# Performance work log

Hardware: AMD Instinct MI355X
Metric: run time of the kernel (lower is better)

The kernel has to match this reference:

```python
import jax, jax.numpy as jnp
import numpy as np

N, E, D_IN, H, C = 100000, 1600000, 256, 128, 10


def setup_inputs() -> dict:
    key = jax.random.key(0)
    ks = jax.random.split(key, 12)
    x = jax.random.normal(ks[0], (N, D_IN), dtype=jnp.float32)
    edge_index = jax.random.randint(ks[1], (2, E), 0, N, dtype=jnp.int64)
    reranker_scores = jax.random.normal(ks[2], (N,), dtype=jnp.float32)
    s_in = 1.0 / np.sqrt(D_IN)
    s_h = 1.0 / np.sqrt(H)
    # SAGEConv: lin_l applies to aggregated neighbors (with bias), lin_r to root (no bias)
    W_l = jax.random.uniform(ks[3], (H, D_IN), jnp.float32, -s_in, s_in)
    b_l = jax.random.uniform(ks[4], (H,), jnp.float32, -s_in, s_in)
    W_r = jax.random.uniform(ks[5], (H, D_IN), jnp.float32, -s_in, s_in)
    W_res = jax.random.uniform(ks[6], (H, D_IN), jnp.float32, -s_in, s_in)
    b_res = jax.random.uniform(ks[7], (H,), jnp.float32, -s_in, s_in)
    W_score = jax.random.uniform(ks[8], (1, H), jnp.float32, -s_h, s_h)
    b_score = jax.random.uniform(ks[9], (1,), jnp.float32, -s_h, s_h)
    W_crit = jax.random.uniform(ks[10], (C, H), jnp.float32, -s_h, s_h)
    b_crit = jax.random.uniform(ks[11], (C,), jnp.float32, -s_h, s_h)
    alpha = jnp.float32(0.65)
    return {"x": x, "edge_index": edge_index, "reranker_scores": reranker_scores,
            "W_l": W_l, "b_l": b_l, "W_r": W_r, "W_res": W_res, "b_res": b_res,
            "W_score": W_score, "b_score": b_score, "W_crit": W_crit, "b_crit": b_crit,
            "alpha": alpha}


def reference(x, edge_index, reranker_scores, W_l, b_l, W_r, W_res, b_res,
              W_score, b_score, W_crit, b_crit, alpha):
    src, dst = edge_index[0], edge_index[1]
    n = x.shape[0]
    ones = jnp.ones(src.shape[0], dtype=x.dtype)
    deg = jax.ops.segment_sum(ones, dst, num_segments=n)          # [N]
    nbr_sum = jax.ops.segment_sum(x[src], dst, num_segments=n)    # [N, D_IN]
    agg = nbr_sum / jnp.maximum(deg, 1.0)[:, None]                # mean aggregation
    # SAGEConv: lin_l(agg) + lin_r(x); relu; dropout (eval -> identity); residual
    h = jax.nn.relu(agg @ W_l.T + b_l + x @ W_r.T)                # [N, H]
    h = h + (x @ W_res.T + b_res)                                 # residual projection
    gnn_scores = (h @ W_score.T + b_score)[:, 0]                  # [N]
    a = jax.nn.sigmoid(alpha)
    final_scores = a * reranker_scores + (1.0 - a) * gnn_scores
    criterion_logits = h @ W_crit.T + b_crit                      # [N, C]
    return final_scores, criterion_logits
```

## Files before the change

### kernel.cpp

```cpp
#include <hip/hip_runtime.h>
#include <math.h>

#define DIN 256
#define HDIM 128
#define NCRIT 10
#define BSH 9
#define EPB 4096

typedef __bf16 bf16;
typedef bf16 bf16x8 __attribute__((ext_vector_type(8)));
typedef float f32x4 __attribute__((ext_vector_type(4)));
typedef float f32x2 __attribute__((ext_vector_type(2)));

static inline size_t alignup(size_t x, size_t a) { return (x + a - 1) & ~(a - 1); }

__device__ inline float bflo(unsigned v) { return __uint_as_float(v << 16); }
__device__ inline float bfhi(unsigned v) { return __uint_as_float(v & 0xffff0000u); }

__device__ inline bf16x8 cvt8(float4 v0, float4 v1) {
    bf16x8 w;
    w[0] = (bf16)v0.x; w[1] = (bf16)v0.y; w[2] = (bf16)v0.z; w[3] = (bf16)v0.w;
    w[4] = (bf16)v1.x; w[5] = (bf16)v1.y; w[6] = (bf16)v1.z; w[7] = (bf16)v1.w;
    return w;
}

__device__ inline void gl_lds16(const void* g, void* l) {
    __builtin_amdgcn_global_load_lds(
        (const __attribute__((address_space(1))) unsigned*)g,
        (__attribute__((address_space(3))) unsigned*)l, 16, 0, 0);
}

__global__ __launch_bounds__(256) void k_bucket2(
    const int* __restrict__ src, const int* __restrict__ dst, int E,
    int* __restrict__ bcnt, int2* __restrict__ bpool, int capb, int nB,
    const float* __restrict__ Wl, const float* __restrict__ Wr,
    const float* __restrict__ Wres,
    const float* __restrict__ wscore, const float* __restrict__ wcrit,
    const float* __restrict__ bres, const float* __restrict__ bscore,
    const float* __restrict__ bcrit,
    bf16* __restrict__ WcatT, float* __restrict__ cq)
{
    int t = threadIdx.x;
    int b = blockIdx.x;
    if (b < 64) {
        int base = (b * 256 + t) * 4;
        int r = base >> 8;
        int c0 = base & 255;
        const float* W = (r < 128) ? Wl : Wr;
        float4 v = *(const float4*)&W[(size_t)(r & 127) * 256 + c0];
        bf16 o[4] = {(bf16)v.x, (bf16)v.y, (bf16)v.z, (bf16)v.w};
        char* d = (char*)WcatT + ((((size_t)(c0 >> 3) * 272 + r) << 4) + ((c0 & 7) << 1));
        *(uint2*)d = *(const uint2*)o;
        return;
    } else if (b < 80) {
        int q = b - 64;
        int k = t;
        float s = 0.f;
        if (q < 11) {
            const float* wepi = (q == 0) ? wscore : &wcrit[(size_t)(q - 1) * HDIM];
            for (int c = 0; c < HDIM; ++c)
                s += wepi[c] * Wres[(size_t)c * 256 + k];
        }
        char* d = (char*)WcatT + ((((size_t)(k >> 3) * 272 + 256 + q) << 4) + ((k & 7) << 1));
        *(bf16*)d = (bf16)s;
        return;
    } else if (b == 80) {
        if (t < 11) {
            const float* wepi = (t == 0) ? wscore : &wcrit[(size_t)(t - 1) * HDIM];
            float s = 0.f;
            for (int c = 0; c < HDIM; ++c) s += bres[c] * wepi[c];
            cq[t] = s + ((t == 0) ? bscore[0] : bcrit[t - 1]);
        }
        return;
    }

    __shared__ int lcnt[256], lbase[256], lcur[256], gbase[256];
    __shared__ int2 stage[EPB];

    int blk = b - 81;
    int base = blk * EPB;
    int m = min(EPB, E - base);
    if (m <= 0) return;

    lcnt[t] = 0;
    __syncthreads();
    for (int i = t; i < m; i += 256)
        atomicAdd(&lcnt[dst[base + i] >> BSH], 1);
    __syncthreads();
    int c0 = lcnt[t];
    for (int d = 1; d < 256; d <<= 1) {
        int a0 = lcnt[t];
        int b0 = (t >= d) ? lcnt[t - d] : 0;
        __syncthreads();
        lcnt[t] = a0 + b0;
        __syncthreads();
    }
    int e0 = lcnt[t] - c0;
    lbase[t] = e0;
    lcur[t] = e0;
    if (t < nB && c0 > 0) gbase[t] = atomicAdd(&bcnt[t * 16], c0);
    __syncthreads();
    for (int i = t; i < m; i += 256) {
        int s2 = src[base + i], d = dst[base + i];
        int bk = d >> BSH;
        int pos = atomicAdd(&lcur[bk], 1);
        stage[pos] = make_int2(s2, d);
    }
    __syncthreads();
    int wv = t >> 6, lane = t & 63;
    for (int bk = wv; bk < nB; bk += 4) {
        int lb = lbase[bk];
        int cb = lcnt[bk] - lb;
        if (cb == 0) continue;
        int gb = gbase[bk];
        int2* dstp = bpool + (size_t)bk * capb + gb;
        for (int j = lane; j < cb && gb + j < capb; j += 64)
            dstp[j] = stage[lb + j];
    }
}

__global__ __launch_bounds__(256) void k_fin(const int* __restrict__ bcnt,
                                             const int2* __restrict__ bpool, int capb,
                                             int n, int* __restrict__ off,
                                             int* __restrict__ cnt, int* __restrict__ sidx) {
    __shared__ int lcnt[512], lcur[512];
    int b = blockIdx.x, t = threadIdx.x;
    int m = min(bcnt[b * 16], capb);
    const int2* ep = bpool + (size_t)b * capb;

    lcnt[t] = 0; lcnt[t + 256] = 0;
    __syncthreads();
    for (int i = t; i < m; i += 256) {
        int2 e = ep[i];
        atomicAdd(&lcnt[e.y & 511], 1);
    }
    __syncthreads();
    int c0 = lcnt[t], c1 = lcnt[t + 256];
    int p0 = (c0 + 3) & ~3, p1 = (c1 + 3) & ~3;
    __syncthreads();
    lcnt[t] = p0; lcnt[t + 256] = p1;
    __syncthreads();
    for (int d = 1; d < 512; d <<= 1) {
        int a0 = lcnt[t], a1 = lcnt[t + 256];
        int b0 = (t >= d) ? lcnt[t - d] : 0;
        int b1 = ((t + 256) >= d) ? lcnt[t + 256 - d] : 0;
        __syncthreads();
        lcnt[t] = a0 + b0; lcnt[t + 256] = a1 + b1;
        __syncthreads();
    }
    int e0 = lcnt[t] - p0, e1 = lcnt[t + 256] - p1;
    int nbase = b << BSH;
    int sbase = b * capb;
    lcur[t] = e0; lcur[t + 256] = e1;
    int n0 = nbase + t, n1 = nbase + t + 256;
    if (n0 < n) { off[n0] = sbase + e0; cnt[n0] = c0; }
    if (n1 < n) { off[n1] = sbase + e1; cnt[n1] = c1; }
    __syncthreads();
    for (int i = t; i < m; i += 256) {
        int2 e = ep[i];
        int pos = atomicAdd(&lcur[e.y & 511], 1);
        sidx[sbase + pos] = e.x;
    }
}

__global__ __launch_bounds__(512) void k_gemm(
    const float* __restrict__ x, const bf16* __restrict__ WcatT, int n,
    unsigned char* __restrict__ yq, bf16* __restrict__ z, float* __restrict__ w,
    const float* __restrict__ bl)
{
    __shared__ __align__(16) char smem[147456];
    int t = threadIdx.x;
    int wv = t >> 6, lane = t & 63;
    int l15 = lane & 15, kq = lane >> 4;

    {
        int cbase0 = wv * 64;
        #pragma unroll
        for (int i = 0; i < 17; i++) {
            int cbase = i * 512 + cbase0;
            gl_lds16((const char*)WcatT + (((size_t)cbase + lane) << 4),
                     smem + ((size_t)cbase << 4));
        }
    }
    __syncthreads();

    char* scr = smem + 139264 + wv * 1024;
    int rrow = lane >> 2, rc4 = (lane & 3) * 4;

    int nTiles = (n + 127) >> 7;
    for (int tile = blockIdx.x; tile < nTiles; tile += gridDim.x) {
        int rowb = tile * 128 + wv * 16;
        int myrow = rowb + l15;
        const float* ap = x + (size_t)(myrow < n ? myrow : (n - 1)) * 256 + kq * 8;

        float4 xa[8], xb[8];
        #pragma unroll
        for (int s = 0; s < 8; s++) {
            xa[s] = *(const float4*)(ap + s * 32);
            xb[s] = *(const float4*)(ap + s * 32 + 4);
        }

        f32x4 acc[17];
        #pragma unroll
        for (int C = 0; C < 17; C++) acc[C] = (f32x4){0.f, 0.f, 0.f, 0.f};

        #pragma unroll
        for (int s = 0; s < 8; s++) {
            bf16x8 afr = cvt8(xa[s], xb[s]);
            int sbase = ((s * 4 + kq) * 272 + l15) << 4;
            #pragma unroll
            for (int C = 0; C < 17; C++) {
                bf16x8 b = *(const bf16x8*)(smem + sbase + C * 256);
                acc[C] = __builtin_amdgcn_mfma_f32_16x16x32_bf16(afr, b, acc[C], 0, 0, 0);
            }
        }

        int gr = rowb + rrow;
        bool ok = gr < n;
        #pragma unroll
        for (int C = 0; C < 17; C++) {
            #pragma unroll
            for (int j = 0; j < 4; j++)
                *(float*)(scr + ((((kq << 2) + j) * 16 + l15) << 2)) = acc[C][j];
            f32x4 vv = *(const f32x4*)(scr + ((rrow * 16 + rc4) << 2));
            if (C < 8) {
                unsigned pk = (unsigned)__builtin_amdgcn_cvt_pk_fp8_f32(vv[0], vv[1], 0, false);
                pk = (unsigned)__builtin_amdgcn_cvt_pk_fp8_f32(vv[2], vv[3], pk, true);
                if (ok) *(unsigned*)(yq + (size_t)gr * 128 + C * 16 + rc4) = pk;
            } else if (C < 16) {
                float4 blv = *(const float4*)&bl[(C - 8) * 16 + rc4];
                bf16 o[4] = {(bf16)(vv[0] + blv.x), (bf16)(vv[1] + blv.y),
                             (bf16)(vv[2] + blv.z), (bf16)(vv[3] + blv.w)};
                if (ok) *(uint2*)((char*)z + (size_t)gr * 256 + (C - 8) * 32 + rc4 * 2) =
                            *(const uint2*)o;
            } else {
                if (ok) *(f32x4*)(w + (size_t)gr * 16 + rc4) = vv;
            }
        }
    }
}

__global__ __launch_bounds__(256) void k_gather(
    const unsigned char* __restrict__ yq, const bf16* __restrict__ z,
    const float* __restrict__ w, const float* __restrict__ cq,
    const int* __restrict__ off, const int* __restrict__ cnt, const int* __restrict__ sidx,
    const float* __restrict__ wscore, const float* __restrict__ wcrit,
    const float* __restrict__ rrs, const float* __restrict__ palpha,
    int n, float* __restrict__ outF, float* __restrict__ outL)
{
    __shared__ bf16 wsb[11 * 128];
    int t = threadIdx.x;
    for (int i = t; i < 11 * 128; i += 256) {
        int q = i >> 7, c = i & 127;
        wsb[i] = (bf16)((q == 0) ? wscore[c] : wcrit[(size_t)(q - 1) * HDIM + c]);
    }
    __syncthreads();

    int node = blockIdx.x * 4 + (t >> 6);
    if (node >= n) return;
    int lane = t & 63, g4 = lane >> 4, c16 = lane & 15;

    uint4 zv = *(const uint4*)((const char*)z + (size_t)node * 256 + c16 * 16);

    const unsigned char* ybase = yq + c16 * 8;
    int beg = off[node], len = cnt[node];
    const int* sp = sidx + beg;

    f32x2 a01 = {0.f, 0.f}, a23 = {0.f, 0.f}, a45 = {0.f, 0.f}, a67 = {0.f, 0.f};
    int e = 0;
    for (; e + 16 <= len; e += 16) {
        int4 iv = *(const int4*)&sp[e + g4 * 4];
        uint2 v0 = *(const uint2*)(ybase + ((size_t)(unsigned)iv.x << 7));
        uint2 v1 = *(const uint2*)(ybase + ((size_t)(unsigned)iv.y << 7));
        uint2 v2 = *(const uint2*)(ybase + ((size_t)(unsigned)iv.z << 7));
        uint2 v3 = *(const uint2*)(ybase + ((size_t)(unsigned)iv.w << 7));
        a01 += __builtin_amdgcn_cvt_pk_f32_fp8(v0.x, false)
             + __builtin_amdgcn_cvt_pk_f32_fp8(v1.x, false)
             + __builtin_amdgcn_cvt_pk_f32_fp8(v2.x, false)
             + __builtin_amdgcn_cvt_pk_f32_fp8(v3.x, false);
        a23 += __builtin_amdgcn_cvt_pk_f32_fp8(v0.x, true)
             + __builtin_amdgcn_cvt_pk_f32_fp8(v1.x, true)
             + __builtin_amdgcn_cvt_pk_f32_fp8(v2.x, true)
             + __builtin_amdgcn_cvt_pk_f32_fp8(v3.x, true);
        a45 += __builtin_amdgcn_cvt_pk_f32_fp8(v0.y, false)
             + __builtin_amdgcn_cvt_pk_f32_fp8(v1.y, false)
             + __builtin_amdgcn_cvt_pk_f32_fp8(v2.y, false)
             + __builtin_amdgcn_cvt_pk_f32_fp8(v3.y, false);
        a67 += __builtin_amdgcn_cvt_pk_f32_fp8(v0.y, true)
             + __builtin_amdgcn_cvt_pk_f32_fp8(v1.y, true)
             + __builtin_amdgcn_cvt_pk_f32_fp8(v2.y, true)
             + __builtin_amdgcn_cvt_pk_f32_fp8(v3.y, true);
    }
    for (; e + 8 <= len; e += 8) {
        int i0 = sp[e + g4];
        int i1 = sp[e + 4 + g4];
        uint2 v0 = *(const uint2*)(ybase + ((size_t)(unsigned)i0 << 7));
        uint2 v1 = *(const uint2*)(ybase + ((size_t)(unsigned)i1 << 7));
        a01 += __builtin_amdgcn_cvt_pk_f32_fp8(v0.x, false)
             + __builtin_amdgcn_cvt_pk_f32_fp8(v1.x, false);
        a23 += __builtin_amdgcn_cvt_pk_f32_fp8(v0.x, true)
             + __builtin_amdgcn_cvt_pk_f32_fp8(v1.x, true);
        a45 += __builtin_amdgcn_cvt_pk_f32_fp8(v0.y, false)
             + __builtin_amdgcn_cvt_pk_f32_fp8(v1.y, false);
        a67 += __builtin_amdgcn_cvt_pk_f32_fp8(v0.y, true)
             + __builtin_amdgcn_cvt_pk_f32_fp8(v1.y, true);
    }
    for (; e < len; e += 4) {
        int slot = e + g4;
        int ii = sp[slot < len ? slot : len - 1];
        uint2 v = *(const uint2*)(ybase + ((size_t)(unsigned)ii << 7));
        if (slot < len) {
            a01 += __builtin_amdgcn_cvt_pk_f32_fp8(v.x, false);
            a23 += __builtin_amdgcn_cvt_pk_f32_fp8(v.x, true);
            a45 += __builtin_amdgcn_cvt_pk_f32_fp8(v.y, false);
            a67 += __builtin_amdgcn_cvt_pk_f32_fp8(v.y, true);
        }
    }
    float a[8] = {a01[0], a01[1], a23[0], a23[1], a45[0], a45[1], a67[0], a67[1]};
    #pragma unroll
    for (int j = 0; j < 8; j++) {
        a[j] += __shfl_xor(a[j], 16, 64);
        a[j] += __shfl_xor(a[j], 32, 64);
    }
    float inv = 1.f / fmaxf((float)len, 1.f);

    float zf[8] = {bflo(zv.x), bfhi(zv.x), bflo(zv.y), bfhi(zv.y),
                   bflo(zv.z), bfhi(zv.z), bflo(zv.w), bfhi(zv.w)};
    float h[8];
    #pragma unroll
    for (int j = 0; j < 8; j++)
        h[j] = fmaxf(a[j] * inv + zf[j], 0.f);

    float p[3];
    #pragma unroll
    for (int qq = 0; qq < 3; qq++) {
        int q = g4 * 3 + qq;
        float s = 0.f;
        if (q < 11) {
            uint4 ww = *(const uint4*)&wsb[q * 128 + c16 * 8];
            s = h[0] * bflo(ww.x) + h[1] * bfhi(ww.x)
              + h[2] * bflo(ww.y) + h[3] * bfhi(ww.y)
              + h[4] * bflo(ww.z) + h[5] * bfhi(ww.z)
              + h[6] * bflo(ww.w) + h[7] * bfhi(ww.w);
        }
        #pragma unroll
        for (int d = 1; d < 16; d <<= 1)
            s += __shfl_xor(s, d, 64);
        p[qq] = s;
    }
    if (c16 == 0) {
        #pragma unroll
        for (int qq = 0; qq < 3; qq++) {
            int q = g4 * 3 + qq;
            if (q >= 11) continue;
            float val = p[qq] + w[(size_t)node * 16 + q] + cq[q];
            if (q == 0) {
                float al = palpha[0];
                float aa = 1.f / (1.f + expf(-al));
                outF[node] = aa * rrs[node] + (1.f - aa) * val;
            } else {
                outL[(size_t)node * NCRIT + q - 1] = val;
            }
        }
    }
}

extern "C" void kernel_launch(void* const* d_in, const int* in_sizes, int n_in,
                              void* d_out, int out_size, void* d_ws, size_t ws_size,
                              hipStream_t stream) {
    const float* x      = (const float*)d_in[0];
    const int*   ei     = (const int*)d_in[1];
    const float* rrs    = (const float*)d_in[2];
    const float* Wl     = (const float*)d_in[3];
    const float* bl     = (const float*)d_in[4];
    const float* Wr     = (const float*)d_in[5];
    const float* Wres   = (const float*)d_in[6];
    const float* bres   = (const float*)d_in[7];
    const float* wscore = (const float*)d_in[8];
    const float* bscore = (const float*)d_in[9];
    const float* wcrit  = (const float*)d_in[10];
    const float* bcrit  = (const float*)d_in[11];
    const float* alpha  = (const float*)d_in[12];

    int N = in_sizes[0] / DIN;
    int E = in_sizes[1] / 2;
    const int* srcv = ei;
    const int* dstv = ei + E;

    int nB = (N + 511) >> BSH;
    int capb = (int)alignup((size_t)(E / (nB > 0 ? nB : 1)) * 2 + 256 + 2048, 4);

    char* p = (char*)d_ws;
    int* bcnt  = (int*)p; p += alignup((size_t)nB * 16 * 4, 256);
    int2* bpool = (int2*)p; p += alignup((size_t)nB * capb * 8, 256);
    int* off   = (int*)p; p += alignup((size_t)N * 4, 256);
    int* cnt   = (int*)p; p += alignup((size_t)N * 4, 256);
    int* sidx  = (int*)p; p += alignup((size_t)nB * capb * 4, 256);
    bf16* WcatT = (bf16*)p; p += alignup((size_t)32 * 272 * 16, 256);
    unsigned char* yq = (unsigned char*)p; p += alignup((size_t)N * HDIM, 256);
    bf16* z    = (bf16*)p; p += alignup((size_t)N * HDIM * 2, 256);
    float* w   = (float*)p; p += alignup((size_t)N * 16 * 4, 256);
    float* cq  = (float*)p; p += 256;

    hipMemsetAsync(bcnt, 0, (size_t)nB * 16 * 4, stream);

    k_bucket2<<<81 + (E + EPB - 1) / EPB, 256, 0, stream>>>(
        srcv, dstv, E, bcnt, bpool, capb, nB, Wl, Wr, Wres, wscore, wcrit,
        bres, bscore, bcrit, WcatT, cq);
    k_fin<<<nB, 256, 0, stream>>>(bcnt, bpool, capb, N, off, cnt, sidx);

    k_gemm<<<256, 512, 0, stream>>>(x, WcatT, N, yq, z, w, bl);

    float* outF = (float*)d_out;
    float* outL = outF + N;
    k_gather<<<(N + 3) / 4, 256, 0, stream>>>(yq, z, w, cq, off, cnt, sidx,
                                              wscore, wcrit, rrs, alpha, N, outF, outL);
}
```

Baseline: 180.1 us.

## Pack bucketed edges into one int and pad neighbor lists with zero row

Edges staged in the bucket pool are packed as (src<<9)|(dst&511) in a single 32-bit word instead of an int2. This halves pool traffic in the bucketing and finalize kernels and halves the LDS staging buffer. Neighbor lists are also padded to multiples of 4 with a dummy index pointing at an extra zeroed yq row, so the gather kernel drops its per-slot masking and clamping tail loop in favor of fixed 8/4 steps. The packing assumes src fits in 23 bits, and the padding adds extra loads of the dummy row.

```diff
diff --git a/kernel.cpp b/kernel.cpp
--- a/kernel.cpp
+++ b/kernel.cpp
@@ -32,7 +32,7 @@
 
 __global__ __launch_bounds__(256) void k_bucket2(
     const int* __restrict__ src, const int* __restrict__ dst, int E,
-    int* __restrict__ bcnt, int2* __restrict__ bpool, int capb, int nB,
+    int* __restrict__ bcnt, int* __restrict__ bpool, int capb, int nB,
     const float* __restrict__ Wl, const float* __restrict__ Wr,
     const float* __restrict__ Wres,
     const float* __restrict__ wscore, const float* __restrict__ wcrit,
@@ -75,7 +75,7 @@
     }
 
     __shared__ int lcnt[256], lbase[256], lcur[256], gbase[256];
-    __shared__ int2 stage[EPB];
+    __shared__ int stage[EPB];
 
     int blk = b - 81;
     int base = blk * EPB;
@@ -104,7 +104,7 @@
         int s2 = src[base + i], d = dst[base + i];
         int bk = d >> BSH;
         int pos = atomicAdd(&lcur[bk], 1);
-        stage[pos] = make_int2(s2, d);
+        stage[pos] = (s2 << BSH) | (d & 511);
     }
     __syncthreads();
     int wv = t >> 6, lane = t & 63;
@@ -113,27 +113,29 @@
         int cb = lcnt[bk] - lb;
         if (cb == 0) continue;
         int gb = gbase[bk];
-        int2* dstp = bpool + (size_t)bk * capb + gb;
+        int* dstp = bpool + (size_t)bk * capb + gb;
         for (int j = lane; j < cb && gb + j < capb; j += 64)
             dstp[j] = stage[lb + j];
     }
 }
 
 __global__ __launch_bounds__(256) void k_fin(const int* __restrict__ bcnt,
-                                             const int2* __restrict__ bpool, int capb,
+                                             const int* __restrict__ bpool, int capb,
                                              int n, int* __restrict__ off,
-                                             int* __restrict__ cnt, int* __restrict__ sidx) {
+                                             int* __restrict__ cnt, int* __restrict__ sidx,
+                                             unsigned char* __restrict__ yq) {
     __shared__ int lcnt[512], lcur[512];
     int b = blockIdx.x, t = threadIdx.x;
     int m = min(bcnt[b * 16], capb);
-    const int2* ep = bpool + (size_t)b * capb;
+    const int* ep = bpool + (size_t)b * capb;
+
+    if (b == 0 && t < 8)
+        *(uint4*)(yq + (size_t)n * 128 + t * 16) = make_uint4(0, 0, 0, 0);
 
     lcnt[t] = 0; lcnt[t + 256] = 0;
     __syncthreads();
-    for (int i = t; i < m; i += 256) {
-        int2 e = ep[i];
-        atomicAdd(&lcnt[e.y & 511], 1);
-    }
+    for (int i = t; i < m; i += 256)
+        atomicAdd(&lcnt[ep[i] & 511], 1);
     __syncthreads();
     int c0 = lcnt[t], c1 = lcnt[t + 256];
     int p0 = (c0 + 3) & ~3, p1 = (c1 + 3) & ~3;
@@ -155,11 +157,13 @@
     int n0 = nbase + t, n1 = nbase + t + 256;
     if (n0 < n) { off[n0] = sbase + e0; cnt[n0] = c0; }
     if (n1 < n) { off[n1] = sbase + e1; cnt[n1] = c1; }
+    for (int j = c0; j < p0; j++) sidx[sbase + e0 + j] = n;
+    for (int j = c1; j < p1; j++) sidx[sbase + e1 + j] = n;
     __syncthreads();
     for (int i = t; i < m; i += 256) {
-        int2 e = ep[i];
-        int pos = atomicAdd(&lcur[e.y & 511], 1);
-        sidx[sbase + pos] = e.x;
+        int e = ep[i];
+        int pos = atomicAdd(&lcur[e & 511], 1);
+        sidx[sbase + pos] = (int)(((unsigned)e) >> BSH);
     }
 }
 
@@ -264,11 +268,12 @@
 
     const unsigned char* ybase = yq + c16 * 8;
     int beg = off[node], len = cnt[node];
+    int lenp = (len + 3) & ~3;
     const int* sp = sidx + beg;
 
     f32x2 a01 = {0.f, 0.f}, a23 = {0.f, 0.f}, a45 = {0.f, 0.f}, a67 = {0.f, 0.f};
     int e = 0;
-    for (; e + 16 <= len; e += 16) {
+    for (; e + 16 <= lenp; e += 16) {
         int4 iv = *(const int4*)&sp[e + g4 * 4];
         uint2 v0 = *(const uint2*)(ybase + ((size_t)(unsigned)iv.x << 7));
         uint2 v1 = *(const uint2*)(ybase + ((size_t)(unsigned)iv.y << 7));
@@ -291,11 +296,10 @@
              + __builtin_amdgcn_cvt_pk_f32_fp8(v2.y, true)
              + __builtin_amdgcn_cvt_pk_f32_fp8(v3.y, true);
     }
-    for (; e + 8 <= len; e += 8) {
-        int i0 = sp[e + g4];
-        int i1 = sp[e + 4 + g4];
-        uint2 v0 = *(const uint2*)(ybase + ((size_t)(unsigned)i0 << 7));
-        uint2 v1 = *(const uint2*)(ybase + ((size_t)(unsigned)i1 << 7));
+    if (lenp & 8) {
+        int2 iv = *(const int2*)&sp[e + g4 * 2];
+        uint2 v0 = *(const uint2*)(ybase + ((size_t)(unsigned)iv.x << 7));
+        uint2 v1 = *(const uint2*)(ybase + ((size_t)(unsigned)iv.y << 7));
         a01 += __builtin_amdgcn_cvt_pk_f32_fp8(v0.x, false)
              + __builtin_amdgcn_cvt_pk_f32_fp8(v1.x, false);
         a23 += __builtin_amdgcn_cvt_pk_f32_fp8(v0.x, true)
@@ -304,17 +308,15 @@
              + __builtin_amdgcn_cvt_pk_f32_fp8(v1.y, false);
         a67 += __builtin_amdgcn_cvt_pk_f32_fp8(v0.y, true)
              + __builtin_amdgcn_cvt_pk_f32_fp8(v1.y, true);
-    }
-    for (; e < len; e += 4) {
-        int slot = e + g4;
-        int ii = sp[slot < len ? slot : len - 1];
-        uint2 v = *(const uint2*)(ybase + ((size_t)(unsigned)ii << 7));
-        if (slot < len) {
-            a01 += __builtin_amdgcn_cvt_pk_f32_fp8(v.x, false);
-            a23 += __builtin_amdgcn_cvt_pk_f32_fp8(v.x, true);
-            a45 += __builtin_amdgcn_cvt_pk_f32_fp8(v.y, false);
-            a67 += __builtin_amdgcn_cvt_pk_f32_fp8(v.y, true);
-        }
+        e += 8;
+    }
+    if (lenp & 4) {
+        int i0 = sp[e + g4];
+        uint2 v = *(const uint2*)(ybase + ((size_t)(unsigned)i0 << 7));
+        a01 += __builtin_amdgcn_cvt_pk_f32_fp8(v.x, false);
+        a23 += __builtin_amdgcn_cvt_pk_f32_fp8(v.x, true);
+        a45 += __builtin_amdgcn_cvt_pk_f32_fp8(v.y, false);
+        a67 += __builtin_amdgcn_cvt_pk_f32_fp8(v.y, true);
     }
     float a[8] = {a01[0], a01[1], a23[0], a23[1], a45[0], a45[1], a67[0], a67[1]};
     #pragma unroll
@@ -392,12 +394,12 @@
 
     char* p = (char*)d_ws;
     int* bcnt  = (int*)p; p += alignup((size_t)nB * 16 * 4, 256);
-    int2* bpool = (int2*)p; p += alignup((size_t)nB * capb * 8, 256);
+    int* bpool = (int*)p; p += alignup((size_t)nB * capb * 4, 256);
     int* off   = (int*)p; p += alignup((size_t)N * 4, 256);
     int* cnt   = (int*)p; p += alignup((size_t)N * 4, 256);
     int* sidx  = (int*)p; p += alignup((size_t)nB * capb * 4, 256);
     bf16* WcatT = (bf16*)p; p += alignup((size_t)32 * 272 * 16, 256);
-    unsigned char* yq = (unsigned char*)p; p += alignup((size_t)N * HDIM, 256);
+    unsigned char* yq = (unsigned char*)p; p += alignup((size_t)(N + 1) * HDIM, 256);
     bf16* z    = (bf16*)p; p += alignup((size_t)N * HDIM * 2, 256);
     float* w   = (float*)p; p += alignup((size_t)N * 16 * 4, 256);
     float* cq  = (float*)p; p += 256;
@@ -407,7 +409,7 @@
     k_bucket2<<<81 + (E + EPB - 1) / EPB, 256, 0, stream>>>(
         srcv, dstv, E, bcnt, bpool, capb, nB, Wl, Wr, Wres, wscore, wcrit,
         bres, bscore, bcrit, WcatT, cq);
-    k_fin<<<nB, 256, 0, stream>>>(bcnt, bpool, capb, N, off, cnt, sidx);
+    k_fin<<<nB, 256, 0, stream>>>(bcnt, bpool, capb, N, off, cnt, sidx, yq);
 
     k_gemm<<<256, 512, 0, stream>>>(x, WcatT, N, yq, z, w, bl);
 
```

Measured after the change: 177.0 us. Within noise of the previous version (-1.7%).
